# Performance work log

Measured on AMD Instinct MI355X. Metric: run time of the kernel, lower is better.

The kernel has to match this reference:

```python
import jax, jax.numpy as jnp
import numpy as np

C = 180        # GatedGraphConv out_channels
L = 6          # num_layers inside GatedGraphConv
NG = 2048      # number of graphs in the batch
FC = 3 * C     # 540
EPS = 1e-5


def setup_inputs() -> dict:
    key = jax.random.key(0)
    ks = jax.random.split(key, 24)
    N, E, F = 50000, 150000, 64
    s = 1.0 / np.sqrt(C)
    inp = {}
    for i in range(3):
        inp[f"x{i+1}"] = jax.random.normal(ks[i], (N, F), jnp.float32)
        inp[f"edge_index{i+1}"] = jax.random.randint(ks[3 + i], (2, E), 0, N)
        inp[f"batch{i+1}"] = jnp.sort(jax.random.randint(ks[6 + i], (N,), 0, NG))
    # GatedGraphConv params (stacked for the 3 graph components)
    inp["conv_W"] = jax.random.normal(ks[9], (3, L, C, C), jnp.float32) * s
    inp["gru_Wih"] = jax.random.normal(ks[10], (3, 3 * C, C), jnp.float32) * s
    inp["gru_Whh"] = jax.random.normal(ks[11], (3, 3 * C, C), jnp.float32) * s
    inp["gru_bih"] = jnp.zeros((3, 3 * C), jnp.float32)
    inp["gru_bhh"] = jnp.zeros((3, 3 * C), jnp.float32)
    # BatchNorm1d (eval mode: running stats)
    inp["bn_gamma"] = jnp.ones((FC,), jnp.float32)
    inp["bn_beta"] = jnp.zeros((FC,), jnp.float32)
    inp["bn_mean"] = jnp.zeros((FC,), jnp.float32)
    inp["bn_var"] = jnp.ones((FC,), jnp.float32)
    # MLP head (torch Linear convention: W is [out, in])
    inp["fc1_W"] = jax.random.normal(ks[12], (FC * 3, FC), jnp.float32) / np.sqrt(FC)
    inp["fc1_b"] = jnp.zeros((FC * 3,), jnp.float32)
    inp["fc2_W"] = jax.random.normal(ks[13], (FC * 3, FC * 3), jnp.float32) / np.sqrt(FC * 3)
    inp["fc2_b"] = jnp.zeros((FC * 3,), jnp.float32)
    inp["fc25_W"] = jax.random.normal(ks[14], (FC, FC * 3), jnp.float32) / np.sqrt(FC * 3)
    inp["fc25_b"] = jnp.zeros((FC,), jnp.float32)
    inp["fc3_W"] = jax.random.normal(ks[15], (3, FC), jnp.float32) / np.sqrt(FC)
    inp["fc3_b"] = jnp.zeros((3,), jnp.float32)
    return inp


def _gated_graph_conv(x, edge_index, W, Wih, Whh, bih, bhh):
    # pad input features up to out_channels (PyG GatedGraphConv behavior)
    h = jnp.pad(x, ((0, 0), (0, C - x.shape[1])))  # [N, C]
    src, dst = edge_index[0], edge_index[1]

    def step(h, Wl):
        m = h @ Wl                                   # [N, C] linear transform
        agg = jnp.zeros_like(h).at[dst].add(m[src])  # scatter-add aggregation
        gi = agg @ Wih.T + bih                       # [N, 3C]
        gh = h @ Whh.T + bhh                         # [N, 3C]
        ir, iz, inn = jnp.split(gi, 3, axis=1)
        hr, hz, hn = jnp.split(gh, 3, axis=1)
        r = jax.nn.sigmoid(ir + hr)
        z = jax.nn.sigmoid(iz + hz)
        n = jnp.tanh(inn + r * hn)
        return (1.0 - z) * n + z * h, None

    h, _ = jax.lax.scan(step, h, W)
    return h


def _pool(h, batch):
    # global_mean_pool: segment mean over graphs
    sums = jax.ops.segment_sum(h, batch, num_segments=NG)
    cnt = jax.ops.segment_sum(jnp.ones((h.shape[0],), h.dtype), batch, num_segments=NG)
    return sums / jnp.maximum(cnt, 1.0)[:, None]


def reference(x1, x2, x3, edge_index1, edge_index2, edge_index3,
              batch1, batch2, batch3, conv_W, gru_Wih, gru_Whh, gru_bih, gru_bhh,
              bn_gamma, bn_beta, bn_mean, bn_var,
              fc1_W, fc1_b, fc2_W, fc2_b, fc25_W, fc25_b, fc3_W, fc3_b):
    xs = (x1, x2, x3)
    eis = (edge_index1, edge_index2, edge_index3)
    bs = (batch1, batch2, batch3)
    pooled = []
    for i in range(3):
        h = _gated_graph_conv(xs[i], eis[i], conv_W[i], gru_Wih[i], gru_Whh[i],
                              gru_bih[i], gru_bhh[i])
        h = jax.nn.relu(h)          # dropout is identity in eval
        pooled.append(_pool(h, bs[i]))
    x = jnp.concatenate(pooled, axis=1)  # [NG, 540]
    x = (x - bn_mean) * jax.lax.rsqrt(bn_var + EPS) * bn_gamma + bn_beta
    x = jax.nn.relu(x @ fc1_W.T + fc1_b)
    x = jax.nn.relu(x @ fc2_W.T + fc2_b)
    x = jax.nn.relu(x @ fc25_W.T + fc25_b)
    return x @ fc3_W.T + fc3_b           # [NG, 3]
```

## Files before the change

kernel.cpp:

```cpp
#include <hip/hip_runtime.h>

typedef unsigned int u32;
typedef unsigned short u16;
typedef __attribute__((ext_vector_type(8))) short bh8;
typedef __attribute__((ext_vector_type(4))) float f32x4;

#define CCH 180
#define LAY 6
#define NGR 2048
#define FIN 64
#define BM 128
#define BN 128
#define BK 20
#define PLANE_ROWS 50049

static __device__ __forceinline__ float sigmoidf_(float x) {
  return 1.0f / (1.0f + expf(-x));
}
static __device__ __forceinline__ u16 f2bf(float x) {
  union { float f; u32 u; } v; v.f = x;
  u32 r = v.u + 0x7FFFu + ((v.u >> 16) & 1u);
  return (u16)(r >> 16);
}
static __device__ __forceinline__ float bf2f(u32 b) {
  union { float f; u32 u; } v; v.u = b << 16;
  return v.f;
}
static __device__ __forceinline__ float unpk(u32 w) {
  return bf2f(w & 0xFFFFu) + bf2f(w >> 16);
}
static __device__ __forceinline__ u32 pk(float x) {
  u16 hi = f2bf(x);
  u16 lo = f2bf(x - bf2f(hi));
  return (u32)hi | ((u32)lo << 16);
}


__global__ void zero_i32_kernel(int* __restrict__ p, int n) {
  int i = blockIdx.x * 256 + threadIdx.x;
  if (i < n) p[i] = 0;
}
__global__ void zero_f32_kernel(float* __restrict__ p, int n) {
  int i = blockIdx.x * 256 + threadIdx.x;
  if (i < n) p[i] = 0.0f;
}

__global__ void pad_x_kernel(const float* __restrict__ x, u32* __restrict__ h, int total) {
  int i = blockIdx.x * 256 + threadIdx.x;
  if (i >= total) return;
  int n = i / CCH;
  int c = i - n * CCH;
  float v = (c < FIN) ? x[(size_t)n * FIN + c] : 0.0f;
  h[i] = pk(v);
}

__global__ void hist_kernel(const int* __restrict__ idx, int* __restrict__ cnt, int n) {
  int i = blockIdx.x * 256 + threadIdx.x;
  if (i < n) atomicAdd(&cnt[idx[i]], 1);
}

__global__ void scan_kernel(const int* __restrict__ deg, int* __restrict__ rowstart,
                            int* __restrict__ cursor, int n) {
  __shared__ int sums[256];
  __shared__ int offs[257];
  int tid = threadIdx.x;
  int per = (n + 255) >> 8;
  int s0 = tid * per;
  int s1 = s0 + per; if (s1 > n) s1 = n;
  int local = 0;
  for (int i = s0; i < s1; ++i) local += deg[i];
  sums[tid] = local;
  __syncthreads();
  if (tid == 0) {
    int r = 0;
    for (int i = 0; i < 256; ++i) { offs[i] = r; r += sums[i]; }
    offs[256] = r;
  }
  __syncthreads();
  int run = offs[tid];
  for (int i = s0; i < s1; ++i) {
    int d = deg[i];
    rowstart[i] = run;
    cursor[i] = run;
    run += d;
  }
  if (tid == 0) rowstart[n] = offs[256];
}

__global__ void fill_kernel(const int* __restrict__ ei, int* __restrict__ cursor,
                            int* __restrict__ srclist, int E) {
  int e = blockIdx.x * 256 + threadIdx.x;
  if (e >= E) return;
  int d = ei[E + e];
  int p = atomicAdd(&cursor[d], 1);
  srclist[p] = ei[e];
}

__global__ void scatter_kernel(const u32* __restrict__ h, const int* __restrict__ rowstart,
                               const int* __restrict__ srclist, u32* __restrict__ out, int N) {
  int n = blockIdx.x * 4 + (threadIdx.x >> 6);
  int lane = threadIdx.x & 63;
  if (n >= N) return;
  int s = rowstart[n], e = rowstart[n + 1];
  float a0 = 0.f, a1 = 0.f, a2 = 0.f;
  for (int i = s; i < e; ++i) {
    const u32* row = h + (size_t)srclist[i] * CCH;
    a0 += unpk(row[lane]);
    a1 += unpk(row[64 + lane]);
    if (lane < 52) a2 += unpk(row[128 + lane]);
  }
  u32* o = out + (size_t)n * CCH;
  o[lane] = pk(a0);
  o[64 + lane] = pk(a1);
  if (lane < 52) o[128 + lane] = pk(a2);
}

__global__ void fill_whh_kernel(const float* __restrict__ Whh_c, float* __restrict__ wc) {
  int cl = blockIdx.y;
  int idx = blockIdx.x * 256 + threadIdx.x;
  if (idx >= 180 * 540) return;
  int k = idx / 540;
  int jj = idx - k * 540;
  int dcol = (jj < 360) ? jj : jj + 180;
  wc[((size_t)cl * 360 + 180 + k) * 720 + dcol] = Whh_c[(size_t)jj * 180 + k];
}

__global__ void wt_build_gru_kernel(const float* __restrict__ wcomb, u32* __restrict__ wt) {
  int i = blockIdx.x * 256 + threadIdx.x;
  if (i >= LAY * 768 * 384) return;
  int l = i / (768 * 384);
  int r = i - l * (768 * 384);
  int c = r / 384, k = r - c * 384;
  int g = c & 3, j = c >> 2;
  float v = 0.0f;
  if (j < 180) {
    int sc = g * 180 + j;
    if (k < 180) v = wcomb[((size_t)l * 360 + k) * 720 + sc];
    else if (k >= 192 && k < 372) v = wcomb[((size_t)l * 360 + 180 + (k - 192)) * 720 + sc];
  }
  wt[i] = pk(v);
}

__global__ void wt_mlp_build_kernel(const float* __restrict__ W, int outR, int inR,
                                    int outPad, int kPad, u32* __restrict__ dst) {
  int i = blockIdx.x * 256 + threadIdx.x;
  if (i >= outPad * kPad) return;
  int col = i / kPad, k = i - col * kPad;
  float v = (col < outR && k < inR) ? W[(size_t)col * inR + k] : 0.0f;
  dst[i] = pk(v);
}

__global__ __launch_bounds__(256) void gemm_bt_kernel(
    const float* __restrict__ A, int lda, long long sAz,
    const float* __restrict__ Bt, int ldb, long long sBz,
    float* __restrict__ Cb, int ldc, long long sCz,
    int M, int Ncols, int K) {
  __shared__ float As[BK][BM + 4];
  __shared__ float Bs[BK][BN + 4];
  int z = blockIdx.z;
  A  += (size_t)z * sAz;
  Bt += (size_t)z * sBz;
  Cb += (size_t)z * sCz;
  int bm = blockIdx.x * BM, bn = blockIdx.y * BN;
  int tid = threadIdx.x;
  int tr = tid >> 4, tc = tid & 15;
  float acc[8][8] = {};
  int lrow = tid >> 1;
  int lkh = (tid & 1) * 10;
  for (int k0 = 0; k0 < K; k0 += BK) {
    {
      int grow = bm + lrow;
      bool ok = (grow < M);
      const float* src = A + (size_t)grow * lda + k0 + lkh;
      #pragma unroll
      for (int i = 0; i < 10; ++i)
        As[lkh + i][lrow] = ok ? src[i] : 0.0f;
    }
    {
      int gcol = bn + lrow;
      bool ok = (gcol < Ncols);
      const float* src = Bt + (size_t)gcol * ldb + k0 + lkh;
      #pragma unroll
      for (int i = 0; i < 10; ++i)
        Bs[lkh + i][lrow] = ok ? src[i] : 0.0f;
    }
    __syncthreads();
    #pragma unroll 5
    for (int kk = 0; kk < BK; ++kk) {
      float4 a0 = *(const float4*)&As[kk][tr * 4];
      float4 a1 = *(const float4*)&As[kk][64 + tr * 4];
      float4 b0 = *(const float4*)&Bs[kk][tc * 4];
      float4 b1 = *(const float4*)&Bs[kk][64 + tc * 4];
      float av[8] = {a0.x, a0.y, a0.z, a0.w, a1.x, a1.y, a1.z, a1.w};
      float bv[8] = {b0.x, b0.y, b0.z, b0.w, b1.x, b1.y, b1.z, b1.w};
      #pragma unroll
      for (int i = 0; i < 8; ++i)
        #pragma unroll
        for (int j = 0; j < 8; ++j)
          acc[i][j] += av[i] * bv[j];
    }
    __syncthreads();
  }
  #pragma unroll
  for (int ih = 0; ih < 2; ++ih)
    #pragma unroll
    for (int i = 0; i < 4; ++i) {
      int r = bm + ih * 64 + tr * 4 + i;
      if (r >= M) continue;
      #pragma unroll
      for (int jh = 0; jh < 2; ++jh) {
        int c0 = bn + jh * 64 + tc * 4;
        if (c0 >= Ncols) continue;
        float4 v;
        v.x = acc[ih * 4 + i][jh * 4 + 0];
        v.y = acc[ih * 4 + i][jh * 4 + 1];
        v.z = acc[ih * 4 + i][jh * 4 + 2];
        v.w = acc[ih * 4 + i][jh * 4 + 3];
        *(float4*)&Cb[(size_t)r * ldc + c0] = v;
      }
    }
}

__global__ __launch_bounds__(256, 2) void gru_fused_kernel(
    const u32* __restrict__ hs, const u32* __restrict__ hp,
    const u32* __restrict__ wt, const float* __restrict__ bih,
    const float* __restrict__ bhh, u32* __restrict__ hnew, int N) {
  __shared__ __align__(16) char smem[128 * 132 * 4];
  u16* Ah = (u16*)smem;
  u16* Al = Ah + 4096;
  u16* Bh = Al + 4096;
  u16* Bl = Bh + 4096;
  int bm = blockIdx.x * BM;
  int bn = blockIdx.y;
  int tid = threadIdx.x;
  int wid = tid >> 6, lane = tid & 63;
  int quad = lane >> 4, l16 = lane & 15;
  int rh = (wid & 1) << 6;
  int ch = (wid >> 1) << 6;
  f32x4 acc[4][4] = {};

  for (int ks = 0; ks < 12; ++ks) {
    const u32* ap = (ks < 6) ? hs : hp;
    int koff = ((ks < 6) ? ks : ks - 6) * 32;
    #pragma unroll
    for (int i = 0; i < 4; ++i) {
      int v = tid + i * 256;
      int rc = v >> 3, qq = v & 7;
      uint4 w = *(const uint4*)(ap + (size_t)(bm + rc) * CCH + koff + qq * 4);
      u32 h0 = (w.x & 0xFFFFu) | (w.y << 16);
      u32 h1 = (w.z & 0xFFFFu) | (w.w << 16);
      u32 l0 = (w.x >> 16) | (w.y & 0xFFFF0000u);
      u32 l1 = (w.z >> 16) | (w.w & 0xFFFF0000u);
      int d = (((qq >> 1) << 7) | rc) * 8 + (qq & 1) * 4;
      *(uint2*)&Ah[d] = make_uint2(h0, h1);
      *(uint2*)&Al[d] = make_uint2(l0, l1);
    }
    #pragma unroll
    for (int i = 0; i < 4; ++i) {
      int v = tid + i * 256;
      int rc = v >> 3, qq = v & 7;
      uint4 w = *(const uint4*)(wt + (size_t)(bn * 128 + rc) * 384 + ks * 32 + qq * 4);
      u32 h0 = (w.x & 0xFFFFu) | (w.y << 16);
      u32 h1 = (w.z & 0xFFFFu) | (w.w << 16);
      u32 l0 = (w.x >> 16) | (w.y & 0xFFFF0000u);
      u32 l1 = (w.z >> 16) | (w.w & 0xFFFF0000u);
      int d = (((qq >> 1) << 7) | rc) * 8 + (qq & 1) * 4;
      *(uint2*)&Bh[d] = make_uint2(h0, h1);
      *(uint2*)&Bl[d] = make_uint2(l0, l1);
    }
    __syncthreads();
    bh8 afh[4], afl[4], bfh[4], bfl[4];
    #pragma unroll
    for (int t = 0; t < 4; ++t) {
      int ra = ((quad << 7) + rh + (t << 4) + l16) << 3;
      afh[t] = *(const bh8*)&Ah[ra];
      afl[t] = *(const bh8*)&Al[ra];
      int rb = ((quad << 7) + ch + (t << 4) + l16) << 3;
      bfh[t] = *(const bh8*)&Bh[rb];
      bfl[t] = *(const bh8*)&Bl[rb];
    }
    #pragma unroll
    for (int i2 = 0; i2 < 4; ++i2)
      #pragma unroll
      for (int j2 = 0; j2 < 4; ++j2) {
        acc[i2][j2] = __builtin_amdgcn_mfma_f32_16x16x32_bf16(afh[i2], bfh[j2], acc[i2][j2], 0, 0, 0);
        acc[i2][j2] = __builtin_amdgcn_mfma_f32_16x16x32_bf16(afh[i2], bfl[j2], acc[i2][j2], 0, 0, 0);
        acc[i2][j2] = __builtin_amdgcn_mfma_f32_16x16x32_bf16(afl[i2], bfh[j2], acc[i2][j2], 0, 0, 0);
      }
    __syncthreads();
  }

  float* T2 = (float*)smem;
  #pragma unroll
  for (int i2 = 0; i2 < 4; ++i2)
    #pragma unroll
    for (int j2 = 0; j2 < 4; ++j2) {
      int col = ch + (j2 << 4) + l16;
      int rb = rh + (i2 << 4) + (quad << 2);
      #pragma unroll
      for (int rg = 0; rg < 4; ++rg)
        T2[(size_t)(rb + rg) * 132 + col] = acc[i2][j2][rg];
    }
  __syncthreads();
  #pragma unroll
  for (int s = 0; s < 16; ++s) {
    int idx = s * 256 + tid;
    int row = idx >> 5, jj = idx & 31;
    int j = bn * 32 + jj;
    int grow = bm + row;
    if (j < 180 && grow < N) {
      float4 g4 = *(const float4*)&T2[(size_t)row * 132 + (jj << 2)];
      float rpre = g4.x + bih[j] + bhh[j];
      float zpre = g4.y + bih[180 + j] + bhh[180 + j];
      float inn  = g4.z + bih[360 + j];
      float hnn  = g4.w + bhh[360 + j];
      float r = sigmoidf_(rpre);
      float z = sigmoidf_(zpre);
      float nn = tanhf(inn + r * hnn);
      float hprev = unpk(hp[(size_t)grow * CCH + j]);
      float hv = (1.0f - z) * nn + z * hprev;
      hnew[(size_t)grow * CCH + j] = pk(hv);
    }
  }
}

__global__ __launch_bounds__(256, 2) void mlp_mfma_kernel(
    const u32* __restrict__ A, int aStride, const u32* __restrict__ wt, int wStride,
    const float* __restrict__ bias, u32* __restrict__ Out, int oStride,
    int Ncols, int nks, int relu) {
  __shared__ __align__(16) char smem[32768];
  u16* Ah = (u16*)smem;
  u16* Al = Ah + 4096;
  u16* Bh = Al + 4096;
  u16* Bl = Bh + 4096;
  int bm = blockIdx.x * BM;
  int bn = blockIdx.y;
  int tid = threadIdx.x;
  int wid = tid >> 6, lane = tid & 63;
  int quad = lane >> 4, l16 = lane & 15;
  int rh = (wid & 1) << 6;
  int ch = (wid >> 1) << 6;
  f32x4 acc[4][4] = {};

  for (int ks = 0; ks < nks; ++ks) {
    int koff = ks * 32;
    #pragma unroll
    for (int i = 0; i < 4; ++i) {
      int v = tid + i * 256;
      int rc = v >> 3, qq = v & 7;
      uint4 w = *(const uint4*)(A + (size_t)(bm + rc) * aStride + koff + qq * 4);
      u32 h0 = (w.x & 0xFFFFu) | (w.y << 16);
      u32 h1 = (w.z & 0xFFFFu) | (w.w << 16);
      u32 l0 = (w.x >> 16) | (w.y & 0xFFFF0000u);
      u32 l1 = (w.z >> 16) | (w.w & 0xFFFF0000u);
      int d = (((qq >> 1) << 7) | rc) * 8 + (qq & 1) * 4;
      *(uint2*)&Ah[d] = make_uint2(h0, h1);
      *(uint2*)&Al[d] = make_uint2(l0, l1);
    }
    #pragma unroll
    for (int i = 0; i < 4; ++i) {
      int v = tid + i * 256;
      int rc = v >> 3, qq = v & 7;
      uint4 w = *(const uint4*)(wt + (size_t)(bn * 128 + rc) * wStride + koff + qq * 4);
      u32 h0 = (w.x & 0xFFFFu) | (w.y << 16);
      u32 h1 = (w.z & 0xFFFFu) | (w.w << 16);
      u32 l0 = (w.x >> 16) | (w.y & 0xFFFF0000u);
      u32 l1 = (w.z >> 16) | (w.w & 0xFFFF0000u);
      int d = (((qq >> 1) << 7) | rc) * 8 + (qq & 1) * 4;
      *(uint2*)&Bh[d] = make_uint2(h0, h1);
      *(uint2*)&Bl[d] = make_uint2(l0, l1);
    }
    __syncthreads();
    bh8 afh[4], afl[4], bfh[4], bfl[4];
    #pragma unroll
    for (int t = 0; t < 4; ++t) {
      int ra = ((quad << 7) + rh + (t << 4) + l16) << 3;
      afh[t] = *(const bh8*)&Ah[ra];
      afl[t] = *(const bh8*)&Al[ra];
      int rb = ((quad << 7) + ch + (t << 4) + l16) << 3;
      bfh[t] = *(const bh8*)&Bh[rb];
      bfl[t] = *(const bh8*)&Bl[rb];
    }
    #pragma unroll
    for (int i2 = 0; i2 < 4; ++i2)
      #pragma unroll
      for (int j2 = 0; j2 < 4; ++j2) {
        acc[i2][j2] = __builtin_amdgcn_mfma_f32_16x16x32_bf16(afh[i2], bfh[j2], acc[i2][j2], 0, 0, 0);
        acc[i2][j2] = __builtin_amdgcn_mfma_f32_16x16x32_bf16(afh[i2], bfl[j2], acc[i2][j2], 0, 0, 0);
        acc[i2][j2] = __builtin_amdgcn_mfma_f32_16x16x32_bf16(afl[i2], bfh[j2], acc[i2][j2], 0, 0, 0);
      }
    __syncthreads();
  }
  #pragma unroll
  for (int i2 = 0; i2 < 4; ++i2)
    #pragma unroll
    for (int j2 = 0; j2 < 4; ++j2) {
      int gc = bn * 128 + ch + (j2 << 4) + l16;
      if (gc >= Ncols) continue;
      float b = bias[gc];
      #pragma unroll
      for (int rg = 0; rg < 4; ++rg) {
        int grow = bm + rh + (i2 << 4) + (quad << 2) + rg;
        float v = acc[i2][j2][rg] + b;
        if (relu) v = fmaxf(v, 0.f);
        Out[(size_t)grow * oStride + gc] = pk(v);
      }
    }
}


__global__ void pool_kernel(const u32* __restrict__ h, const int* __restrict__ gstart,
                            float* __restrict__ pooled, int coff) {
  int g = blockIdx.x;
  int c = threadIdx.x;
  if (c >= CCH) return;
  int s = gstart[g], e = gstart[g + 1];
  float acc = 0.f;
  for (int n = s; n < e; ++n) acc += fmaxf(unpk(h[(size_t)n * CCH + c]), 0.f);
  pooled[(size_t)g * 540 + coff + c] = acc / fmaxf((float)(e - s), 1.0f);
}

__global__ void bn_pack_kernel(const float* __restrict__ p, const float* __restrict__ mean,
                               const float* __restrict__ var, const float* __restrict__ gamma,
                               const float* __restrict__ beta, u32* __restrict__ xn, int total) {
  int i = blockIdx.x * 256 + threadIdx.x;
  if (i >= total) return;
  int g = i / 540;
  int c = i - g * 540;
  float sc = gamma[c] / sqrtf(var[c] + 1e-5f);
  float v = (p[i] - mean[c]) * sc + beta[c];
  xn[(size_t)g * 544 + c] = pk(v);
}

__global__ void fc3_kernel(const u32* __restrict__ X, const float* __restrict__ W,
                           const float* __restrict__ b, float* __restrict__ out) {
  int g = blockIdx.x;
  int lane = threadIdx.x;
  const u32* x = X + (size_t)g * 544;
  for (int j = 0; j < 3; ++j) {
    const float* w = W + (size_t)j * 540;
    float s = 0.f;
    for (int i = lane; i < 540; i += 64) s += unpk(x[i]) * w[i];
    #pragma unroll
    for (int o = 32; o > 0; o >>= 1) s += __shfl_down(s, o);
    if (lane == 0) out[(size_t)g * 3 + j] = s + b[j];
  }
}


extern "C" void kernel_launch(void* const* d_in, const int* in_sizes, int n_in,
                              void* d_out, int out_size, void* d_ws, size_t ws_size,
                              hipStream_t stream) {
  (void)n_in; (void)out_size; (void)ws_size;
  const float* xs[3]   = {(const float*)d_in[0], (const float*)d_in[3], (const float*)d_in[6]};
  const int*   eis[3]  = {(const int*)d_in[1], (const int*)d_in[4], (const int*)d_in[7]};
  const int*   bats[3] = {(const int*)d_in[2], (const int*)d_in[5], (const int*)d_in[8]};
  const float* convW = (const float*)d_in[9];
  const float* Wih   = (const float*)d_in[10];
  const float* Whh   = (const float*)d_in[11];
  const float* bih   = (const float*)d_in[12];
  const float* bhh   = (const float*)d_in[13];
  const float* bng   = (const float*)d_in[14];
  const float* bnb   = (const float*)d_in[15];
  const float* bnm   = (const float*)d_in[16];
  const float* bnv   = (const float*)d_in[17];
  const float* fc1W  = (const float*)d_in[18];
  const float* fc1b  = (const float*)d_in[19];
  const float* fc2W  = (const float*)d_in[20];
  const float* fc2b  = (const float*)d_in[21];
  const float* fc25W = (const float*)d_in[22];
  const float* fc25b = (const float*)d_in[23];
  const float* fc3W  = (const float*)d_in[24];
  const float* fc3b  = (const float*)d_in[25];

  const int N = in_sizes[0] / FIN;
  const int E = in_sizes[1] / 2;

  char* p = (char*)d_ws;
  auto alloc = [&](size_t bytes) -> char* {
    char* r = p;
    p += (bytes + 255) & ~(size_t)255;
    return r;
  };
  const size_t PLANE = (size_t)PLANE_ROWS * CCH * 4;
  u32* P0 = (u32*)alloc(PLANE);
  u32* P1 = (u32*)alloc(PLANE);
  u32* P2 = (u32*)alloc(PLANE);
  float* pooled = (float*)alloc((size_t)NGR * 540 * 4);
  int* rowstart = (int*)alloc((size_t)(N + 1) * 4);
  int* srclist  = (int*)alloc((size_t)E * 4);
  int* gstart   = (int*)alloc((size_t)(NGR + 1) * 4);
  int* gcnt     = (int*)alloc((size_t)NGR * 4);

  float* wcomb = (float*)P2;
  int* cursor  = (int*)((char*)P2 + 6815744);
  u32* wtf1  = (u32*)P0;
  u32* wtf2  = wtf1 + (size_t)1664 * 544;
  u32* wtf25 = wtf2 + (size_t)1664 * 1632;
  u32* xn = (u32*)P1;
  u32* t1 = xn + (size_t)NGR * 544;
  u32* t2 = t1 + (size_t)NGR * 1632;
  u32* t3 = t2 + (size_t)NGR * 1632;

  const int rowBlocks = (N + BM - 1) / BM;

  for (int comp = 0; comp < 3; ++comp) {
    pad_x_kernel<<<(N * CCH + 255) / 256, 256, 0, stream>>>(xs[comp], P1, N * CCH);

    zero_f32_kernel<<<(LAY * 360 * 720 + 255) / 256, 256, 0, stream>>>(wcomb, LAY * 360 * 720);
    {
      dim3 grid((180 + BM - 1) / BM, (540 + BN - 1) / BN, LAY);
      gemm_bt_kernel<<<grid, 256, 0, stream>>>(
          convW + (size_t)comp * LAY * 180 * 180, 180, 180LL * 180,
          Wih + (size_t)comp * 540 * 180, 180, 0,
          wcomb, 720, 360LL * 720, 180, 540, 180);
      dim3 g2((180 * 540 + 255) / 256, LAY);
      fill_whh_kernel<<<g2, 256, 0, stream>>>(Whh + (size_t)comp * 540 * 180, wcomb);
    }
    u32* wtg = (u32*)d_in[comp * 3];
    wt_build_gru_kernel<<<(LAY * 768 * 384 + 255) / 256, 256, 0, stream>>>(wcomb, wtg);

    zero_i32_kernel<<<(N + 255) / 256, 256, 0, stream>>>(cursor, N);
    hist_kernel<<<(E + 255) / 256, 256, 0, stream>>>(eis[comp] + E, cursor, E);
    scan_kernel<<<1, 256, 0, stream>>>(cursor, rowstart, cursor, N);
    fill_kernel<<<(E + 255) / 256, 256, 0, stream>>>(eis[comp], cursor, srclist, E);

    const float* bih_c = bih + (size_t)comp * 540;
    const float* bhh_c = bhh + (size_t)comp * 540;
    for (int l = 0; l < LAY; ++l) {
      const u32* hp = (l & 1) ? P2 : P1;
      u32* hn = (l & 1) ? P1 : P2;
      scatter_kernel<<<(N + 3) / 4, 256, 0, stream>>>(hp, rowstart, srclist, P0, N);
      dim3 gg(rowBlocks, 6);
      gru_fused_kernel<<<gg, 256, 0, stream>>>(P0, hp, wtg + (size_t)l * 768 * 384,
                                               bih_c, bhh_c, hn, N);
    }
    zero_i32_kernel<<<(NGR + 255) / 256, 256, 0, stream>>>(gcnt, NGR);
    hist_kernel<<<(N + 255) / 256, 256, 0, stream>>>(bats[comp], gcnt, N);
    scan_kernel<<<1, 256, 0, stream>>>(gcnt, gstart, gcnt, NGR);
    pool_kernel<<<NGR, 192, 0, stream>>>(P1, gstart, pooled, comp * CCH);
  }

  wt_mlp_build_kernel<<<(1664 * 544 + 255) / 256, 256, 0, stream>>>(fc1W, 1620, 540, 1664, 544, wtf1);
  wt_mlp_build_kernel<<<(1664 * 1632 + 255) / 256, 256, 0, stream>>>(fc2W, 1620, 1620, 1664, 1632, wtf2);
  wt_mlp_build_kernel<<<(640 * 1632 + 255) / 256, 256, 0, stream>>>(fc25W, 540, 1620, 640, 1632, wtf25);

  bn_pack_kernel<<<(NGR * 540 + 255) / 256, 256, 0, stream>>>(pooled, bnm, bnv, bng, bnb, xn, NGR * 540);
  {
    dim3 g1(NGR / BM, 13);
    mlp_mfma_kernel<<<g1, 256, 0, stream>>>(xn, 544, wtf1, 544, fc1b, t1, 1632, 1620, 17, 1);
    mlp_mfma_kernel<<<g1, 256, 0, stream>>>(t1, 1632, wtf2, 1632, fc2b, t2, 1632, 1620, 51, 1);
    dim3 g3(NGR / BM, 5);
    mlp_mfma_kernel<<<g3, 256, 0, stream>>>(t2, 1632, wtf25, 1632, fc25b, t3, 544, 540, 51, 1);
    fc3_kernel<<<NGR, 64, 0, stream>>>(t3, fc3W, fc3b, (float*)d_out);
  }
}
```

Measured before the change: 4.473 ms.

## Do GRU epilogue in registers via DPP, shrink LDS, remap blocks for reuse

```diff
diff --git a/kernel.cpp b/kernel.cpp
--- a/kernel.cpp
+++ b/kernel.cpp
@@ -33,6 +33,10 @@
   u16 hi = f2bf(x);
   u16 lo = f2bf(x - bf2f(hi));
   return (u32)hi | ((u32)lo << 16);
+}
+template <int T>
+static __device__ __forceinline__ float qbroad(float v) {
+  return __int_as_float(__builtin_amdgcn_mov_dpp(__float_as_int(v), T * 85, 0xF, 0xF, true));
 }
 
 
@@ -139,6 +143,14 @@
     else if (k >= 192 && k < 372) v = wcomb[((size_t)l * 360 + 180 + (k - 192)) * 720 + sc];
   }
   wt[i] = pk(v);
+}
+
+__global__ void bias4_build_kernel(const float* __restrict__ bih, const float* __restrict__ bhh,
+                                   float4* __restrict__ b4) {
+  int j = blockIdx.x * 64 + threadIdx.x;
+  if (j < CCH)
+    b4[j] = make_float4(bih[j] + bhh[j], bih[180 + j] + bhh[180 + j],
+                        bih[360 + j], bhh[360 + j]);
 }
 
 __global__ void wt_mlp_build_kernel(const float* __restrict__ W, int outR, int inR,
@@ -221,17 +233,32 @@
     }
 }
 
-__global__ __launch_bounds__(256, 2) void gru_fused_kernel(
+__global__ __launch_bounds__(256, 4) void gru_fused_kernel(
     const u32* __restrict__ hs, const u32* __restrict__ hp,
-    const u32* __restrict__ wt, const float* __restrict__ bih,
-    const float* __restrict__ bhh, u32* __restrict__ hnew, int N) {
-  __shared__ __align__(16) char smem[128 * 132 * 4];
-  u16* Ah = (u16*)smem;
+    const u32* __restrict__ wt, const float4* __restrict__ bias4,
+    u32* __restrict__ hnew, int N) {
+  __shared__ __align__(16) u16 smem[4 * 4096];
+  u16* Ah = smem;
   u16* Al = Ah + 4096;
   u16* Bh = Al + 4096;
   u16* Bl = Bh + 4096;
-  int bm = blockIdx.x * BM;
-  int bn = blockIdx.y;
+
+  int R = (N + 127) >> 7;
+  int b = blockIdx.x;
+  int full = (R >> 3) * 48;
+  int bm_t, bn;
+  if (b < full) {
+    int g = b / 48, w = b - g * 48;
+    bn = w >> 3;
+    bm_t = (g << 3) + (w & 7);
+  } else {
+    int rem = R & 7;
+    int b2 = b - full;
+    bn = b2 / rem;
+    bm_t = ((R >> 3) << 3) + (b2 - bn * rem);
+  }
+  int bm = bm_t << 7;
+
   int tid = threadIdx.x;
   int wid = tid >> 6, lane = tid & 63;
   int quad = lane >> 4, l16 = lane & 15;
@@ -290,38 +317,32 @@
     __syncthreads();
   }
 
-  float* T2 = (float*)smem;
+  bool writer = ((l16 & 3) == 0);
   #pragma unroll
   for (int i2 = 0; i2 < 4; ++i2)
     #pragma unroll
     for (int j2 = 0; j2 < 4; ++j2) {
-      int col = ch + (j2 << 4) + l16;
-      int rb = rh + (i2 << 4) + (quad << 2);
-      #pragma unroll
-      for (int rg = 0; rg < 4; ++rg)
-        T2[(size_t)(rb + rg) * 132 + col] = acc[i2][j2][rg];
-    }
-  __syncthreads();
-  #pragma unroll
-  for (int s = 0; s < 16; ++s) {
-    int idx = s * 256 + tid;
-    int row = idx >> 5, jj = idx & 31;
-    int j = bn * 32 + jj;
-    int grow = bm + row;
-    if (j < 180 && grow < N) {
-      float4 g4 = *(const float4*)&T2[(size_t)row * 132 + (jj << 2)];
-      float rpre = g4.x + bih[j] + bhh[j];
-      float zpre = g4.y + bih[180 + j] + bhh[180 + j];
-      float inn  = g4.z + bih[360 + j];
-      float hnn  = g4.w + bhh[360 + j];
-      float r = sigmoidf_(rpre);
-      float z = sigmoidf_(zpre);
-      float nn = tanhf(inn + r * hnn);
-      float hprev = unpk(hp[(size_t)grow * CCH + j]);
-      float hv = (1.0f - z) * nn + z * hprev;
-      hnew[(size_t)grow * CCH + j] = pk(hv);
-    }
-  }
+      int colbase = bn * 128 + ch + (j2 << 4) + (l16 & ~3);
+      int j = colbase >> 2;
+      #pragma unroll
+      for (int rg = 0; rg < 4; ++rg) {
+        float v = acc[i2][j2][rg];
+        float g0 = qbroad<0>(v);
+        float g1 = qbroad<1>(v);
+        float g2 = qbroad<2>(v);
+        float g3 = qbroad<3>(v);
+        int grow = bm + rh + (i2 << 4) + (quad << 2) + rg;
+        if (writer && j < CCH && grow < N) {
+          float4 b4 = bias4[j];
+          float r = sigmoidf_(g0 + b4.x);
+          float z = sigmoidf_(g1 + b4.y);
+          float nn = tanhf(g2 + b4.z + r * (g3 + b4.w));
+          float hprev = unpk(hp[(size_t)grow * CCH + j]);
+          float hv = (1.0f - z) * nn + z * hprev;
+          hnew[(size_t)grow * CCH + j] = pk(hv);
+        }
+      }
+    }
 }
 
 __global__ __launch_bounds__(256, 2) void mlp_mfma_kernel(
@@ -487,6 +508,7 @@
   u32* P1 = (u32*)alloc(PLANE);
   u32* P2 = (u32*)alloc(PLANE);
   float* pooled = (float*)alloc((size_t)NGR * 540 * 4);
+  float4* bias4 = (float4*)alloc((size_t)CCH * 16);
   int* rowstart = (int*)alloc((size_t)(N + 1) * 4);
   int* srclist  = (int*)alloc((size_t)E * 4);
   int* gstart   = (int*)alloc((size_t)(NGR + 1) * 4);
@@ -519,21 +541,20 @@
     }
     u32* wtg = (u32*)d_in[comp * 3];
     wt_build_gru_kernel<<<(LAY * 768 * 384 + 255) / 256, 256, 0, stream>>>(wcomb, wtg);
+    bias4_build_kernel<<<3, 64, 0, stream>>>(bih + (size_t)comp * 540,
+                                             bhh + (size_t)comp * 540, bias4);
 
     zero_i32_kernel<<<(N + 255) / 256, 256, 0, stream>>>(cursor, N);
     hist_kernel<<<(E + 255) / 256, 256, 0, stream>>>(eis[comp] + E, cursor, E);
     scan_kernel<<<1, 256, 0, stream>>>(cursor, rowstart, cursor, N);
     fill_kernel<<<(E + 255) / 256, 256, 0, stream>>>(eis[comp], cursor, srclist, E);
 
-    const float* bih_c = bih + (size_t)comp * 540;
-    const float* bhh_c = bhh + (size_t)comp * 540;
     for (int l = 0; l < LAY; ++l) {
       const u32* hp = (l & 1) ? P2 : P1;
       u32* hn = (l & 1) ? P1 : P2;
       scatter_kernel<<<(N + 3) / 4, 256, 0, stream>>>(hp, rowstart, srclist, P0, N);
-      dim3 gg(rowBlocks, 6);
-      gru_fused_kernel<<<gg, 256, 0, stream>>>(P0, hp, wtg + (size_t)l * 768 * 384,
-                                               bih_c, bhh_c, hn, N);
+      gru_fused_kernel<<<rowBlocks * 6, 256, 0, stream>>>(P0, hp, wtg + (size_t)l * 768 * 384,
+                                                          bias4, hn, N);
     }
     zero_i32_kernel<<<(NGR + 255) / 256, 256, 0, stream>>>(gcnt, NGR);
     hist_kernel<<<(N + 255) / 256, 256, 0, stream>>>(bats[comp], gcnt, N);
```

New measurement: 5.033 ms. +12.5%, slower.
